# Optimization experiments

Measured on AMD Instinct MI355X. Metric: run time of the kernel, lower is better.

The kernel has to match this reference:

```python
import jax, jax.numpy as jnp
import numpy as np

N_NODES = 50000
N_EDGES = 800000
D = 128


def setup_inputs() -> dict:
    key = jax.random.key(0)
    ks = jax.random.split(key, 8)
    scale = 1.0 / np.sqrt(D)
    return {
        "x": jax.random.normal(ks[0], (N_NODES, D), jnp.float32),
        "src": jax.random.randint(ks[1], (N_EDGES,), 0, N_NODES, jnp.int64 if jax.config.jax_enable_x64 else jnp.int32),
        "dst": jax.random.randint(ks[2], (N_EDGES,), 0, N_NODES, jnp.int64 if jax.config.jax_enable_x64 else jnp.int32),
        "W_self0": jax.random.normal(ks[3], (D, D), jnp.float32) * scale,
        "W_neigh0": jax.random.normal(ks[4], (D, D), jnp.float32) * scale,
        "b0": jnp.zeros((D,), jnp.float32),
        "W_self1": jax.random.normal(ks[5], (D, D), jnp.float32) * scale,
        "W_neigh1": jax.random.normal(ks[6], (D, D), jnp.float32) * scale,
        "b1": jnp.zeros((D,), jnp.float32),
    }


def _sage_conv(h, src, dst, W_self, W_neigh, b, n_nodes):
    # mean aggregation over incoming edges (DGL copy_u + mean; isolated nodes -> 0)
    msg = h[src]                                             # [E, d]
    agg = jax.ops.segment_sum(msg, dst, num_segments=n_nodes)  # [N, d]
    deg = jax.ops.segment_sum(jnp.ones((src.shape[0],), h.dtype), dst, num_segments=n_nodes)
    h_neigh = agg / jnp.maximum(deg, 1.0)[:, None]
    return h @ W_self + h_neigh @ W_neigh + b


def reference(x, src, dst, W_self0, W_neigh0, b0, W_self1, W_neigh1, b1):
    n = x.shape[0]
    h = jax.nn.relu(_sage_conv(x, src, dst, W_self0, W_neigh0, b0, n))
    h = jax.nn.relu(_sage_conv(h, src, dst, W_self1, W_neigh1, b1, n))
    # torch F.normalize(p=2, dim=1): x / max(||x||_2, eps)
    norm = jnp.sqrt(jnp.sum(h * h, axis=1, keepdims=True))
    return h / jnp.maximum(norm, 1e-12)
```

## Files before the change

kernel.cpp:

```cpp
#include <hip/hip_runtime.h>

#define NN 50000
#define D 128
#define BM 32

typedef unsigned int uint;
typedef unsigned short ushort;
typedef __attribute__((ext_vector_type(8))) short bf16x8;
typedef __attribute__((ext_vector_type(4))) float f32x4;

static __device__ __forceinline__ ushort f2bf(float f) {
    uint u = __float_as_uint(f);
    u = (u + 0x7FFFu + ((u >> 16) & 1u)) >> 16;
    return (ushort)u;
}

#define ADD8(a, u)                                                  \
    {                                                               \
        a[0] += __uint_as_float((u).x << 16);                       \
        a[1] += __uint_as_float((u).x & 0xFFFF0000u);               \
        a[2] += __uint_as_float((u).y << 16);                       \
        a[3] += __uint_as_float((u).y & 0xFFFF0000u);               \
        a[4] += __uint_as_float((u).z << 16);                       \
        a[5] += __uint_as_float((u).z & 0xFFFF0000u);               \
        a[6] += __uint_as_float((u).w << 16);                       \
        a[7] += __uint_as_float((u).w & 0xFFFF0000u);               \
    }

static __device__ __forceinline__ int ladr(int r, int ch) {
    return r * D + (((ch) ^ (r & 7)) << 3);
}

__global__ void k_cvt(const float* __restrict__ x, ushort* __restrict__ xb, int n8) {
    int t = blockIdx.x * blockDim.x + threadIdx.x;
    if (t >= n8) return;
    const float4* p = reinterpret_cast<const float4*>(x) + (size_t)t * 2;
    const float4 v0 = p[0], v1 = p[1];
    uint4 u;
    u.x = (uint)f2bf(v0.x) | ((uint)f2bf(v0.y) << 16);
    u.y = (uint)f2bf(v0.z) | ((uint)f2bf(v0.w) << 16);
    u.z = (uint)f2bf(v1.x) | ((uint)f2bf(v1.y) << 16);
    u.w = (uint)f2bf(v1.z) | ((uint)f2bf(v1.w) << 16);
    reinterpret_cast<uint4*>(xb)[t] = u;
}

__global__ void k_wpack(const float* __restrict__ W0, const float* __restrict__ W1,
                        const float* __restrict__ W2, const float* __restrict__ W3,
                        ushort* __restrict__ P) {
    int o = blockIdx.x * 256 + threadIdx.x;
    if (o >= 65536) return;
    const int mat = o >> 14;
    const int idx = o & 16383;
    const int kt = idx >> 12;
    const int n  = (idx >> 5) & 127;
    const int ks = idx & 31;
    const float* W = (mat == 0) ? W0 : (mat == 1) ? W1 : (mat == 2) ? W2 : W3;
    P[o] = f2bf(W[(kt * 32 + ks) * D + n]);
}

__global__ void k_hist(const int* __restrict__ dst, int* __restrict__ hist, int E) {
    int e = blockIdx.x * blockDim.x + threadIdx.x;
    if (e < E) atomicAdd(&hist[dst[e]], 1);
}

__global__ __launch_bounds__(256) void k_bsum(const int* __restrict__ hist,
                                              int* __restrict__ bsum, int n) {
    const int t = threadIdx.x;
    const int i0 = blockIdx.x * 512 + t * 2;
    int s = 0;
    if (i0 < n) s += hist[i0];
    if (i0 + 1 < n) s += hist[i0 + 1];
    #pragma unroll
    for (int o = 1; o < 64; o <<= 1) s += __shfl_xor(s, o);
    __shared__ int wsum[4];
    if ((t & 63) == 0) wsum[t >> 6] = s;
    __syncthreads();
    if (t == 0) bsum[blockIdx.x] = wsum[0] + wsum[1] + wsum[2] + wsum[3];
}

__global__ __launch_bounds__(128) void k_bscan(int* __restrict__ bsum, int nb) {
    const int t = threadIdx.x;
    const int lane = t & 63, w = t >> 6;
    int v = (t < nb) ? bsum[t] : 0;
    int inc = v;
    #pragma unroll
    for (int o = 1; o < 64; o <<= 1) { int u = __shfl_up(inc, o); if (lane >= o) inc += u; }
    __shared__ int wsum[2];
    if (lane == 63) wsum[w] = inc;
    __syncthreads();
    int off = (w == 1) ? wsum[0] : 0;
    if (t < nb) bsum[t] = off + inc - v;
}

__global__ __launch_bounds__(256) void k_apply(const int* __restrict__ hist,
        const int* __restrict__ bsum, int* __restrict__ row_off,
        int* __restrict__ cursor, int n, int E) {
    const int t = threadIdx.x;
    const int i0 = blockIdx.x * 512 + t * 2;
    const int v0 = (i0 < n) ? hist[i0] : 0;
    const int v1 = (i0 + 1 < n) ? hist[i0 + 1] : 0;
    const int s = v0 + v1;
    const int lane = t & 63, w = t >> 6;
    int inc = s;
    #pragma unroll
    for (int o = 1; o < 64; o <<= 1) { int u = __shfl_up(inc, o); if (lane >= o) inc += u; }
    __shared__ int wsum[4], woff[4];
    if (lane == 63) wsum[w] = inc;
    __syncthreads();
    if (t == 0) { int r = 0; for (int k = 0; k < 4; ++k) { woff[k] = r; r += wsum[k]; } }
    __syncthreads();
    const int ex = bsum[blockIdx.x] + woff[w] + (inc - s);
    if (i0 < n)     { row_off[i0] = ex;          cursor[i0] = ex; }
    if (i0 + 1 < n) { row_off[i0 + 1] = ex + v0; cursor[i0 + 1] = ex + v0; }
    if (blockIdx.x == 0 && t == 0) row_off[n] = E;
}

__global__ void k_fill(const int* __restrict__ src, const int* __restrict__ dst,
                       int* __restrict__ cursor, int* __restrict__ csr, int E) {
    int e = blockIdx.x * blockDim.x + threadIdx.x;
    if (e < E) {
        int p = atomicAdd(&cursor[dst[e]], 1);
        csr[p] = src[e];
    }
}

template<bool NORM>
__global__ __launch_bounds__(512, 4) void k_sage(
    const ushort* __restrict__ hb,
    const int* __restrict__ csr, const int* __restrict__ row_off,
    const ushort* __restrict__ Wps, const ushort* __restrict__ Wpn,
    const float* __restrict__ bias, ushort* __restrict__ outb,
    float* __restrict__ out, int n, int E)
{
    __shared__ __align__(16) ushort hsb[BM * D];
    __shared__ __align__(16) ushort hnb[BM * D];
    __shared__ float outt[BM * 132];
    const int row0 = blockIdx.x * BM;
    const int tid = threadIdx.x;
    const int l = tid & 63;
    const int w = tid >> 6;

    {
        const int r = tid >> 4;
        const int ch = tid & 15;
        const int g = row0 + r;
        uint4 u = make_uint4(0u, 0u, 0u, 0u);
        if (g < n) u = *reinterpret_cast<const uint4*>(hb + (size_t)g * D + ch * 8);
        *reinterpret_cast<uint4*>(&hsb[ladr(r, ch)]) = u;
    }

    {
        const int r = tid >> 4;
        const int ql = tid & 15;
        const int g = row0 + r;
        int i = 0, e = 0;
        if (g < n) { i = row_off[g]; e = row_off[g + 1]; }
        const float invd = (e > i) ? 1.0f / (float)(e - i) : 0.0f;
        float a[8];
        #pragma unroll
        for (int j = 0; j < 8; ++j) a[j] = 0.f;
        const size_t off = (size_t)(ql * 8);
        for (; i + 3 < e; i += 4) {
            const int s0 = csr[i], s1 = csr[i + 1], s2 = csr[i + 2], s3 = csr[i + 3];
            const uint4 u0 = *reinterpret_cast<const uint4*>(hb + (size_t)s0 * D + off);
            const uint4 u1 = *reinterpret_cast<const uint4*>(hb + (size_t)s1 * D + off);
            const uint4 u2 = *reinterpret_cast<const uint4*>(hb + (size_t)s2 * D + off);
            const uint4 u3 = *reinterpret_cast<const uint4*>(hb + (size_t)s3 * D + off);
            ADD8(a, u0); ADD8(a, u1); ADD8(a, u2); ADD8(a, u3);
        }
        for (; i < e; ++i) {
            const int s0 = csr[i];
            const uint4 u0 = *reinterpret_cast<const uint4*>(hb + (size_t)s0 * D + off);
            ADD8(a, u0);
        }
        uint4 u;
        u.x = (uint)f2bf(a[0] * invd) | ((uint)f2bf(a[1] * invd) << 16);
        u.y = (uint)f2bf(a[2] * invd) | ((uint)f2bf(a[3] * invd) << 16);
        u.z = (uint)f2bf(a[4] * invd) | ((uint)f2bf(a[5] * invd) << 16);
        u.w = (uint)f2bf(a[6] * invd) | ((uint)f2bf(a[7] * invd) << 16);
        *reinterpret_cast<uint4*>(&hnb[ladr(r, ql)]) = u;
    }
    __syncthreads();

    {
        const int mt = w >> 2;
        const int ntA = (w & 3) * 2;
        const int rA = mt * 16 + (l & 15);
        const int kg = l >> 4;
        f32x4 acc0 = {0.f, 0.f, 0.f, 0.f};
        f32x4 acc1 = {0.f, 0.f, 0.f, 0.f};
        #pragma unroll
        for (int kt = 0; kt < 4; ++kt) {
            const int kc = kt * 4 + kg;
            const bf16x8 as = *reinterpret_cast<const bf16x8*>(&hsb[ladr(rA, kc)]);
            const bf16x8 an = *reinterpret_cast<const bf16x8*>(&hnb[ladr(rA, kc)]);
            const size_t wo0 = (size_t)(kt * 128 + ntA * 16 + (l & 15)) * 32 + kg * 8;
            const size_t wo1 = wo0 + 16 * 32;
            const bf16x8 bs0 = *reinterpret_cast<const bf16x8*>(Wps + wo0);
            const bf16x8 bn0 = *reinterpret_cast<const bf16x8*>(Wpn + wo0);
            const bf16x8 bs1 = *reinterpret_cast<const bf16x8*>(Wps + wo1);
            const bf16x8 bn1 = *reinterpret_cast<const bf16x8*>(Wpn + wo1);
            acc0 = __builtin_amdgcn_mfma_f32_16x16x32_bf16(as, bs0, acc0, 0, 0, 0);
            acc0 = __builtin_amdgcn_mfma_f32_16x16x32_bf16(an, bn0, acc0, 0, 0, 0);
            acc1 = __builtin_amdgcn_mfma_f32_16x16x32_bf16(as, bs1, acc1, 0, 0, 0);
            acc1 = __builtin_amdgcn_mfma_f32_16x16x32_bf16(an, bn1, acc1, 0, 0, 0);
        }
        const int c0 = ntA * 16 + (l & 15);
        const float bv0 = bias[c0], bv1 = bias[c0 + 16];
        #pragma unroll
        for (int i2 = 0; i2 < 4; ++i2) {
            const int rr = mt * 16 + kg * 4 + i2;
            outt[rr * 132 + c0]      = fmaxf(acc0[i2] + bv0, 0.f);
            outt[rr * 132 + c0 + 16] = fmaxf(acc1[i2] + bv1, 0.f);
        }
    }
    __syncthreads();

    {
        const int r = tid >> 4;
        const int c = (tid & 15) * 8;
        const int g = row0 + r;
        float4 v0 = *reinterpret_cast<const float4*>(&outt[r * 132 + c]);
        float4 v1 = *reinterpret_cast<const float4*>(&outt[r * 132 + c + 4]);
        if (!NORM) {
            if (g < n) {
                uint4 u;
                u.x = (uint)f2bf(v0.x) | ((uint)f2bf(v0.y) << 16);
                u.y = (uint)f2bf(v0.z) | ((uint)f2bf(v0.w) << 16);
                u.z = (uint)f2bf(v1.x) | ((uint)f2bf(v1.y) << 16);
                u.w = (uint)f2bf(v1.z) | ((uint)f2bf(v1.w) << 16);
                *reinterpret_cast<uint4*>(outb + (size_t)g * D + c) = u;
            }
        } else {
            float ssq = v0.x * v0.x + v0.y * v0.y + v0.z * v0.z + v0.w * v0.w
                      + v1.x * v1.x + v1.y * v1.y + v1.z * v1.z + v1.w * v1.w;
            #pragma unroll
            for (int o = 1; o < 16; o <<= 1) ssq += __shfl_xor(ssq, o);
            const float scale = 1.0f / fmaxf(sqrtf(ssq), 1e-12f);
            if (g < n) {
                v0.x *= scale; v0.y *= scale; v0.z *= scale; v0.w *= scale;
                v1.x *= scale; v1.y *= scale; v1.z *= scale; v1.w *= scale;
                *reinterpret_cast<float4*>(out + (size_t)g * D + c)     = v0;
                *reinterpret_cast<float4*>(out + (size_t)g * D + c + 4) = v1;
            }
        }
    }
}

extern "C" void kernel_launch(void* const* d_in, const int* in_sizes, int n_in,
                              void* d_out, int out_size, void* d_ws, size_t ws_size,
                              hipStream_t stream) {
    const float* x   = (const float*)d_in[0];
    const int*   src = (const int*)d_in[1];
    const int*   dst = (const int*)d_in[2];
    const float* Ws0 = (const float*)d_in[3];
    const float* Wn0 = (const float*)d_in[4];
    const float* b0  = (const float*)d_in[5];
    const float* Ws1 = (const float*)d_in[6];
    const float* Wn1 = (const float*)d_in[7];
    const float* b1  = (const float*)d_in[8];
    float* out = (float*)d_out;
    const int E = in_sizes[1];

    ushort* xb     = (ushort*)d_ws;
    ushort* h1b    = xb + (size_t)NN * D;
    ushort* Wp     = h1b + (size_t)NN * D;
    int*    hist   = (int*)(Wp + 65536);
    int*    bsum   = hist + NN;
    int*    row_off= bsum + 128;
    int*    cursor = row_off + NN + 1;
    int*    csr    = cursor + NN;

    ushort* Wps0 = Wp;
    ushort* Wpn0 = Wp + 16384;
    ushort* Wps1 = Wp + 32768;
    ushort* Wpn1 = Wp + 49152;

    const int nb = (NN + 511) / 512;

    k_cvt<<<(NN * D / 8 + 255) / 256, 256, 0, stream>>>(x, xb, NN * D / 8);
    k_wpack<<<256, 256, 0, stream>>>(Ws0, Wn0, Ws1, Wn1, Wp);

    hipMemsetAsync(hist, 0, (size_t)NN * sizeof(int), stream);
    k_hist<<<(E + 255) / 256, 256, 0, stream>>>(dst, hist, E);
    k_bsum<<<nb, 256, 0, stream>>>(hist, bsum, NN);
    k_bscan<<<1, 128, 0, stream>>>(bsum, nb);
    k_apply<<<nb, 256, 0, stream>>>(hist, bsum, row_off, cursor, NN, E);
    k_fill<<<(E + 255) / 256, 256, 0, stream>>>(src, dst, cursor, csr, E);

    k_sage<false><<<(NN + BM - 1) / BM, 512, 0, stream>>>(
        xb, csr, row_off, Wps0, Wpn0, b0, h1b, nullptr, NN, E);

    k_sage<true><<<(NN + BM - 1) / BM, 512, 0, stream>>>(
        h1b, csr, row_off, Wps1, Wpn1, b1, nullptr, out, NN, E);
}
```

Baseline: 193.7 us.

## Fuse prep kernels and partition histogram/CSR fill atomics by destination slice

Merges bf16 conversion, weight packing and degree histogram into one launch, removing two kernel launches. The histogram and CSR fill now split destination node ids into 8 slices, with each block scanning all edges but only doing atomics for its slice. The goal is to keep each block's atomics on a narrower address range for better L2 locality. The cost is that every edge is read 8 times across slices, and CSR neighbor order within a row changes, which could slightly change float summation order.

```diff
diff --git a/kernel.cpp b/kernel.cpp
--- a/kernel.cpp
+++ b/kernel.cpp
@@ -3,6 +3,7 @@
 #define NN 50000
 #define D 128
 #define BM 32
+#define SL 6250
 
 typedef unsigned int uint;
 typedef unsigned short ushort;
@@ -31,36 +32,43 @@
     return r * D + (((ch) ^ (r & 7)) << 3);
 }
 
-__global__ void k_cvt(const float* __restrict__ x, ushort* __restrict__ xb, int n8) {
-    int t = blockIdx.x * blockDim.x + threadIdx.x;
-    if (t >= n8) return;
-    const float4* p = reinterpret_cast<const float4*>(x) + (size_t)t * 2;
-    const float4 v0 = p[0], v1 = p[1];
-    uint4 u;
-    u.x = (uint)f2bf(v0.x) | ((uint)f2bf(v0.y) << 16);
-    u.y = (uint)f2bf(v0.z) | ((uint)f2bf(v0.w) << 16);
-    u.z = (uint)f2bf(v1.x) | ((uint)f2bf(v1.y) << 16);
-    u.w = (uint)f2bf(v1.z) | ((uint)f2bf(v1.w) << 16);
-    reinterpret_cast<uint4*>(xb)[t] = u;
-}
-
-__global__ void k_wpack(const float* __restrict__ W0, const float* __restrict__ W1,
-                        const float* __restrict__ W2, const float* __restrict__ W3,
-                        ushort* __restrict__ P) {
-    int o = blockIdx.x * 256 + threadIdx.x;
-    if (o >= 65536) return;
-    const int mat = o >> 14;
-    const int idx = o & 16383;
-    const int kt = idx >> 12;
-    const int n  = (idx >> 5) & 127;
-    const int ks = idx & 31;
-    const float* W = (mat == 0) ? W0 : (mat == 1) ? W1 : (mat == 2) ? W2 : W3;
-    P[o] = f2bf(W[(kt * 32 + ks) * D + n]);
-}
-
-__global__ void k_hist(const int* __restrict__ dst, int* __restrict__ hist, int E) {
-    int e = blockIdx.x * blockDim.x + threadIdx.x;
-    if (e < E) atomicAdd(&hist[dst[e]], 1);
+__global__ __launch_bounds__(256) void k_prep(
+    const float* __restrict__ x, ushort* __restrict__ xb,
+    const float* __restrict__ W0, const float* __restrict__ W1,
+    const float* __restrict__ W2, const float* __restrict__ W3,
+    ushort* __restrict__ P,
+    const int* __restrict__ dst, int* __restrict__ hist, int E)
+{
+    const int bid = blockIdx.x;
+    if (bid < 3125) {
+        const int t = bid * 256 + threadIdx.x;
+        const float4* p = reinterpret_cast<const float4*>(x) + (size_t)t * 2;
+        const float4 v0 = p[0], v1 = p[1];
+        uint4 u;
+        u.x = (uint)f2bf(v0.x) | ((uint)f2bf(v0.y) << 16);
+        u.y = (uint)f2bf(v0.z) | ((uint)f2bf(v0.w) << 16);
+        u.z = (uint)f2bf(v1.x) | ((uint)f2bf(v1.y) << 16);
+        u.w = (uint)f2bf(v1.z) | ((uint)f2bf(v1.w) << 16);
+        reinterpret_cast<uint4*>(xb)[t] = u;
+    } else if (bid < 3125 + 256) {
+        const int o = (bid - 3125) * 256 + threadIdx.x;
+        const int mat = o >> 14;
+        const int idx = o & 16383;
+        const int kt = idx >> 12;
+        const int n  = (idx >> 5) & 127;
+        const int ks = idx & 31;
+        const float* W = (mat == 0) ? W0 : (mat == 1) ? W1 : (mat == 2) ? W2 : W3;
+        P[o] = f2bf(W[(kt * 32 + ks) * D + n]);
+    } else {
+        const int hb = bid - (3125 + 256);
+        const int s = hb & 7;
+        const int lo = s * SL, hi = lo + SL;
+        const int bs = hb >> 3;
+        for (int e = bs * 256 + (int)threadIdx.x; e < E; e += 128 * 256) {
+            const int d = dst[e];
+            if (d >= lo && d < hi) atomicAdd(&hist[d], 1);
+        }
+    }
 }
 
 __global__ __launch_bounds__(256) void k_bsum(const int* __restrict__ hist,
@@ -115,12 +123,20 @@
     if (blockIdx.x == 0 && t == 0) row_off[n] = E;
 }
 
-__global__ void k_fill(const int* __restrict__ src, const int* __restrict__ dst,
-                       int* __restrict__ cursor, int* __restrict__ csr, int E) {
-    int e = blockIdx.x * blockDim.x + threadIdx.x;
-    if (e < E) {
-        int p = atomicAdd(&cursor[dst[e]], 1);
-        csr[p] = src[e];
+__global__ __launch_bounds__(256) void k_fill_s(const int* __restrict__ src,
+        const int* __restrict__ dst, int* __restrict__ cursor,
+        int* __restrict__ csr, int E) {
+    const int s = blockIdx.x & 7;
+    const int lo = s * SL, hi = lo + SL;
+    const int bs = blockIdx.x >> 3;
+    const int stride = (gridDim.x >> 3) * 256;
+    for (int e = bs * 256 + (int)threadIdx.x; e < E; e += stride) {
+        const int d = dst[e];
+        const int sv = src[e];
+        if (d >= lo && d < hi) {
+            const int p = atomicAdd(&cursor[d], 1);
+            csr[p] = sv;
+        }
     }
 }
 
@@ -278,15 +294,13 @@
 
     const int nb = (NN + 511) / 512;
 
-    k_cvt<<<(NN * D / 8 + 255) / 256, 256, 0, stream>>>(x, xb, NN * D / 8);
-    k_wpack<<<256, 256, 0, stream>>>(Ws0, Wn0, Ws1, Wn1, Wp);
-
     hipMemsetAsync(hist, 0, (size_t)NN * sizeof(int), stream);
-    k_hist<<<(E + 255) / 256, 256, 0, stream>>>(dst, hist, E);
+    k_prep<<<3125 + 256 + 1024, 256, 0, stream>>>(x, xb, Ws0, Wn0, Ws1, Wn1, Wp,
+                                                  dst, hist, E);
     k_bsum<<<nb, 256, 0, stream>>>(hist, bsum, NN);
     k_bscan<<<1, 128, 0, stream>>>(bsum, nb);
     k_apply<<<nb, 256, 0, stream>>>(hist, bsum, row_off, cursor, NN, E);
-    k_fill<<<(E + 255) / 256, 256, 0, stream>>>(src, dst, cursor, csr, E);
+    k_fill_s<<<1024, 256, 0, stream>>>(src, dst, cursor, csr, E);
 
     k_sage<false><<<(NN + BM - 1) / BM, 512, 0, stream>>>(
         xb, csr, row_off, Wps0, Wpn0, b0, h1b, nullptr, NN, E);
```

Result: faster. 178.1 us (-8.0%).
